# Kernel optimization log

Hardware: AMD Instinct MI355X
Metric: run time of the kernel (lower is better)

## Reference

```python
import jax, jax.numpy as jnp
import numpy as np

GROUPS = 32
EPS = 1e-5


def setup_inputs() -> dict:
    key = jax.random.key(0)
    ks = jax.random.split(key, 6)
    B, H, W, C = 2, 64, 64, 512
    wscale = 0.02  # keep logits in a sane range for softmax
    return {
        "x": jax.random.normal(ks[0], (B, H, W, C), dtype=jnp.float32),
        "gamma": jnp.ones((C,), jnp.float32),
        "beta": jnp.zeros((C,), jnp.float32),
        "wq": jax.random.normal(ks[1], (C, C), dtype=jnp.float32) * wscale,
        "bq": jnp.zeros((C,), jnp.float32),
        "wk": jax.random.normal(ks[2], (C, C), dtype=jnp.float32) * wscale,
        "bk": jnp.zeros((C,), jnp.float32),
        "wv": jax.random.normal(ks[3], (C, C), dtype=jnp.float32) * wscale,
        "bv": jnp.zeros((C,), jnp.float32),
        "wp": jax.random.normal(ks[4], (C, C), dtype=jnp.float32) * wscale,
        "bp": jnp.zeros((C,), jnp.float32),
    }


def _group_norm(x, gamma, beta):
    B, H, W, C = x.shape
    xg = x.reshape(B, H, W, GROUPS, C // GROUPS)
    mean = xg.mean(axis=(1, 2, 4), keepdims=True)
    var = xg.var(axis=(1, 2, 4), keepdims=True)
    xn = ((xg - mean) * jax.lax.rsqrt(var + EPS)).reshape(B, H, W, C)
    return xn * gamma + beta


def reference(x, gamma, beta, wq, bq, wk, bk, wv, bv, wp, bp):
    B, H, W, C = x.shape
    xn = _group_norm(x, gamma, beta)
    # 1x1 convs == per-pixel linear layers
    q = (xn @ wq + bq).reshape(B, H * W, C)
    k = (xn @ wk + bk).reshape(B, H * W, C)
    v = (xn @ wv + bv).reshape(B, H * W, C)
    scale = C ** (-0.5)
    attn = jax.nn.softmax(jnp.einsum("bqc,bkc->bqk", q, k) * scale, axis=-1)
    out = jnp.einsum("bqk,bkc->bqc", attn, v).reshape(B, H, W, C)
    return (out @ wp + bp) + x
```

## Files before the change

### kernel.cpp

```cpp
#include <hip/hip_runtime.h>


typedef __bf16 bf16_t;
typedef __bf16 bf16x8 __attribute__((ext_vector_type(8)));
typedef __bf16 bf16x4 __attribute__((ext_vector_type(4)));
typedef float  f32x4  __attribute__((ext_vector_type(4)));

__device__ __forceinline__ bf16x8 ld8(const bf16_t* p) {
    return *reinterpret_cast<const bf16x8*>(p);
}
__device__ __forceinline__ f32x4 mfma16(bf16x8 a, bf16x8 b, f32x4 c) {
    return __builtin_amdgcn_mfma_f32_16x16x32_bf16(a, b, c, 0, 0, 0);
}
__device__ __forceinline__ void gload16(const bf16_t* gp, bf16_t* lp) {
    __builtin_amdgcn_global_load_lds(
        (const __attribute__((address_space(1))) void*)gp,
        (__attribute__((address_space(3))) void*)lp, 16, 0, 0);
}

#define NPIX 8192
#define C512 512
#define SEQ  4096
#define QSCALE 0.044194173824159216f

__global__ __launch_bounds__(256) void gn_sum_k(const float* __restrict__ x,
                                                float* __restrict__ accum) {
    int bg    = blockIdx.x >> 3;
    int slice = blockIdx.x & 7;
    int b = bg >> 5, g = bg & 31;
    const float* xp = x + (size_t)b * SEQ * C512 + g * 16;
    float s = 0.f, s2 = 0.f;
    #pragma unroll
    for (int pp = 0; pp < 2; pp++) {
        int p = slice * 512 + pp * 256 + threadIdx.x;
        const float4* q = reinterpret_cast<const float4*>(xp + (size_t)p * C512);
        #pragma unroll
        for (int i = 0; i < 4; i++) {
            float4 v = q[i];
            s  += v.x + v.y + v.z + v.w;
            s2 += v.x*v.x + v.y*v.y + v.z*v.z + v.w*v.w;
        }
    }
    #pragma unroll
    for (int off = 32; off >= 1; off >>= 1) {
        s  += __shfl_down(s, off);
        s2 += __shfl_down(s2, off);
    }
    __shared__ float rs[4], rs2[4];
    int wave = threadIdx.x >> 6;
    if ((threadIdx.x & 63) == 0) { rs[wave] = s; rs2[wave] = s2; }
    __syncthreads();
    if (threadIdx.x == 0) {
        float S = rs[0] + rs[1] + rs[2] + rs[3];
        float S2 = rs2[0] + rs2[1] + rs2[2] + rs2[3];
        atomicAdd(&accum[bg * 2],     S);
        atomicAdd(&accum[bg * 2 + 1], S2);
    }
}

__global__ __launch_bounds__(256) void wt_conv_k(const float* wq, const float* wk,
                                                 const float* wv, const float* wp,
                                                 bf16_t* wqkvT, bf16_t* wpT) {
    int y = blockIdx.y;
    const float* w = (y == 0) ? wq : (y == 1) ? wk : (y == 2) ? wv : wp;
    float scale = (y == 0) ? QSCALE : 1.0f;
    int tid = blockIdx.x * 256 + threadIdx.x;
    int n = tid >> 9, k = tid & 511;
    bf16_t val = (bf16_t)(w[(size_t)k * C512 + n] * scale);
    if (y < 3) wqkvT[((size_t)y * C512 + n) * C512 + k] = val;
    else       wpT[(size_t)n * C512 + k] = val;
}

__global__ __launch_bounds__(256) void bias_merge_k(const float* bq, const float* bk,
                                                    const float* bv, float* bqkv) {
    int i = blockIdx.x * 256 + threadIdx.x;
    float v = (i < 512) ? bq[i] * QSCALE : (i < 1024) ? bk[i - 512] : bv[i - 1024];
    bqkv[i] = v;
}

__global__ __launch_bounds__(256) void xn_k(const float* __restrict__ x,
                                            const float* __restrict__ accum,
                                            const float* __restrict__ gamma,
                                            const float* __restrict__ beta,
                                            bf16_t* __restrict__ xn) {
    size_t idx = ((size_t)blockIdx.x * 256 + threadIdx.x) * 4;
    int c = (int)(idx & 511);
    size_t pix = idx >> 9;
    int b = (int)(pix >> 12);
    int g = c >> 4;
    float sum = accum[(b * 32 + g) * 2];
    float ssq = accum[(b * 32 + g) * 2 + 1];
    float mean = sum * (1.f / 65536.f);
    float var  = ssq * (1.f / 65536.f) - mean * mean;
    float rstd = rsqrtf(var + 1e-5f);
    float4 v  = *reinterpret_cast<const float4*>(x + idx);
    float4 gm = *reinterpret_cast<const float4*>(gamma + c);
    float4 bt = *reinterpret_cast<const float4*>(beta + c);
    bf16x4 o;
    o[0] = (bf16_t)((v.x - mean) * rstd * gm.x + bt.x);
    o[1] = (bf16_t)((v.y - mean) * rstd * gm.y + bt.y);
    o[2] = (bf16_t)((v.z - mean) * rstd * gm.z + bt.z);
    o[3] = (bf16_t)((v.w - mean) * rstd * gm.w + bt.w);
    *reinterpret_cast<bf16x4*>(xn + idx) = o;
}

template <int MODE>
__global__ __launch_bounds__(256, 2) void gemm128_k(
        const bf16_t* __restrict__ Aall, const bf16_t* __restrict__ Ball,
        const float* __restrict__ bias, const float* __restrict__ resid,
        void* __restrict__ out0, void* __restrict__ out1,
        void* __restrict__ out2, void* __restrict__ out3,
        float* __restrict__ lsum) {
    constexpr int TM  = (MODE == 3) ? 64 : 128;
    constexpr int ASZ = TM * 32;
    constexpr int ACH = TM / 16;
    constexpr int CPW = (ACH + 8) / 4;
    constexpr int MI  = TM / 32;
    __shared__ bf16_t smem[2 * ASZ + 8192];

    int lane = threadIdx.x & 63;
    int w    = threadIdx.x >> 6;
    int wr   = w >> 1, wc = w & 1;
    int lrow = lane & 15, quad = lane >> 4;
    int bz   = blockIdx.z;

    const bf16_t* A;
    const bf16_t* B;
    size_t lda, ldb;
    int ksteps, kofs = 0, zb = bz, sp = 0;
    if (MODE == 0)      { A = Aall;                         B = Ball;                        lda = 512;  ldb = 512;  ksteps = 16; }
    else if (MODE == 1) { A = Aall + (size_t)bz*SEQ*C512;   B = Ball + (size_t)bz*SEQ*C512;  lda = 512;  ldb = 512;  ksteps = 16; }
    else if (MODE == 2) { zb = bz >> 2; sp = bz & 3;
                          A = Aall + (size_t)zb*SEQ*SEQ;    B = Ball + (size_t)zb*C512*SEQ;  lda = SEQ;  ldb = SEQ;  ksteps = 32; kofs = sp * 1024; }
    else                { A = Aall;                         B = Ball;                        lda = 512;  ldb = 512;  ksteps = 16; }

    int bm = blockIdx.x * TM, bn = blockIdx.y * 128;

    auto stage = [&](int buf, int ks) {
        size_t k0 = (size_t)kofs + (size_t)ks * 32;
        #pragma unroll
        for (int ii = 0; ii < CPW; ii++) {
            int c = w * CPW + ii;
            if (c < ACH) {
                const bf16_t* gpA = A + (size_t)(bm + c * 16 + lrow) * lda + k0 + quad * 8;
                gload16(gpA, &smem[buf * ASZ + c * 512]);
            } else {
                int cb = c - ACH;
                const bf16_t* gpB = B + (size_t)(bn + cb * 16 + lrow) * ldb + k0 + quad * 8;
                gload16(gpB, &smem[2 * ASZ + buf * 4096 + cb * 512]);
            }
        }
    };

    f32x4 acc[MI][4] = {};

    stage(0, 0);

    for (int ks = 0; ks < ksteps; ks++) {
        int cur = ks & 1;
        __syncthreads();
        if (ks + 1 < ksteps) stage(1 - cur, ks + 1);

        const bf16_t* al = &smem[cur * ASZ + (wr * MI) * 512];
        const bf16_t* bl = &smem[2 * ASZ + cur * 4096 + (wc * 4) * 512];
        bf16x8 af[MI], bf[4];
        #pragma unroll
        for (int m = 0; m < MI; m++) af[m] = ld8(al + m * 512 + lane * 8);
        #pragma unroll
        for (int n = 0; n < 4; n++) bf[n] = ld8(bl + n * 512 + lane * 8);
        #pragma unroll
        for (int m = 0; m < MI; m++)
            #pragma unroll
            for (int n = 0; n < 4; n++)
                acc[m][n] = mfma16(af[m], bf[n], acc[m][n]);
    }

    float rs[MI][4];
    if (MODE == 1) {
        #pragma unroll
        for (int m = 0; m < MI; m++)
            #pragma unroll
            for (int i = 0; i < 4; i++) rs[m][i] = 0.f;
    }

    #pragma unroll
    for (int m = 0; m < MI; m++) {
        int rowb = bm + wr * (TM / 2) + m * 16 + quad * 4;
        #pragma unroll
        for (int n = 0; n < 4; n++) {
            int col = bn + wc * 64 + n * 16 + lrow;
            #pragma unroll
            for (int i = 0; i < 4; i++) {
                int row = rowb + i;
                float v = acc[m][n][i];
                if (MODE == 0) {
                    int seg = col >> 9, c = col & 511;
                    bf16_t val = (bf16_t)(v + bias[col]);
                    if (seg == 0) {
                        ((bf16_t*)out0)[(size_t)row * C512 + c] = val;
                    } else if (seg == 1) {
                        ((bf16_t*)out1)[(size_t)row * C512 + c] = val;
                    } else {
                        int b = row >> 12, s = row & 4095;
                        ((bf16_t*)out2)[((size_t)(b * C512 + c)) * SEQ + s] = val;
                    }
                } else if (MODE == 1) {
                    float p = __expf(fminf(v, 20.0f));
                    bf16_t* P = (bf16_t*)out0 + (size_t)bz * SEQ * SEQ;
                    P[(size_t)row * SEQ + col] = (bf16_t)p;
                    rs[m][i] += p;
                } else if (MODE == 2) {
                    bf16_t* Ops = (bf16_t*)((sp == 0) ? out0 : (sp == 1) ? out1
                                          : (sp == 2) ? out2 : out3);
                    Ops[((size_t)zb * SEQ + row) * C512 + col] = (bf16_t)v;
                } else {
                    size_t idx = (size_t)row * C512 + col;
                    ((float*)out0)[idx] = v + bias[col] + resid[idx];
                }
            }
        }
    }

    if (MODE == 1) {
        #pragma unroll
        for (int m = 0; m < MI; m++) {
            #pragma unroll
            for (int i = 0; i < 4; i++) {
                float r = rs[m][i];
                r += __shfl_xor(r, 1);
                r += __shfl_xor(r, 2);
                r += __shfl_xor(r, 4);
                r += __shfl_xor(r, 8);
                if (lrow == 0) {
                    int row = bm + wr * 64 + m * 16 + quad * 4 + i;
                    atomicAdd(&lsum[(size_t)bz * SEQ + row], r);
                }
            }
        }
    }
}

__global__ __launch_bounds__(256) void attn_combine_k(const bf16_t* __restrict__ Op0,
                                                      const bf16_t* __restrict__ Op1,
                                                      const bf16_t* __restrict__ Op2,
                                                      const bf16_t* __restrict__ Op3,
                                                      const float* __restrict__ lsum,
                                                      bf16_t* __restrict__ O) {
    int idx = blockIdx.x * 256 + threadIdx.x;
    int row = idx >> 6;
    int c8  = (idx & 63) << 3;
    float inv = 1.0f / lsum[row];
    size_t base = (size_t)row * C512 + c8;
    bf16x8 o0 = ld8(Op0 + base), o1 = ld8(Op1 + base);
    bf16x8 o2 = ld8(Op2 + base), o3 = ld8(Op3 + base);
    bf16x8 o;
    #pragma unroll
    for (int j = 0; j < 8; j++)
        o[j] = (bf16_t)(((float)o0[j] + (float)o1[j] +
                         (float)o2[j] + (float)o3[j]) * inv);
    *reinterpret_cast<bf16x8*>(O + base) = o;
}

extern "C" void kernel_launch(void* const* d_in, const int* in_sizes, int n_in,
                              void* d_out, int out_size, void* d_ws, size_t ws_size,
                              hipStream_t stream) {
    const float* x     = (const float*)d_in[0];
    const float* gamma = (const float*)d_in[1];
    const float* beta  = (const float*)d_in[2];
    const float* wq = (const float*)d_in[3];  const float* bq = (const float*)d_in[4];
    const float* wk = (const float*)d_in[5];  const float* bk = (const float*)d_in[6];
    const float* wv = (const float*)d_in[7];  const float* bv = (const float*)d_in[8];
    const float* wp = (const float*)d_in[9];  const float* bp = (const float*)d_in[10];
    float* out = (float*)d_out;

    char* ws = (char*)d_ws;
    size_t off = 0;
    float*  bqkv   = (float*)(ws + off);   off += 1536 * sizeof(float);
    float*  lsum   = (float*)(ws + off);   off += (size_t)NPIX * sizeof(float);
    float*  accum  = (float*)(ws + off);   off += 128 * sizeof(float);
    bf16_t* xn     = (bf16_t*)(ws + off);  off += (size_t)NPIX * C512 * 2;
    bf16_t* wqkvT  = (bf16_t*)(ws + off);  off += (size_t)3 * C512 * C512 * 2;
    bf16_t* wpT    = (bf16_t*)(ws + off);  off += (size_t)C512 * C512 * 2;
    bf16_t* Qb     = (bf16_t*)(ws + off);  off += (size_t)NPIX * C512 * 2;
    bf16_t* Kb     = (bf16_t*)(ws + off);  off += (size_t)NPIX * C512 * 2;
    bf16_t* VTb    = (bf16_t*)(ws + off);  off += (size_t)NPIX * C512 * 2;
    bf16_t* Op2    = (bf16_t*)(ws + off);  off += (size_t)NPIX * C512 * 2;
    bf16_t* Op3    = (bf16_t*)(ws + off);  off += (size_t)NPIX * C512 * 2;
    bf16_t* P      = (bf16_t*)(ws + off);  off += (size_t)2 * SEQ * SEQ * 2;
    bf16_t* Ob  = xn;
    bf16_t* Op0 = Qb;
    bf16_t* Op1 = Kb;

    hipMemsetAsync(lsum, 0, (size_t)(NPIX + 128) * sizeof(float), stream);

    gn_sum_k<<<512, 256, 0, stream>>>(x, accum);
    wt_conv_k<<<dim3(1024, 4), 256, 0, stream>>>(wq, wk, wv, wp, wqkvT, wpT);
    bias_merge_k<<<6, 256, 0, stream>>>(bq, bk, bv, bqkv);
    xn_k<<<4096, 256, 0, stream>>>(x, accum, gamma, beta, xn);

    gemm128_k<0><<<dim3(64, 12, 1), 256, 0, stream>>>(
        xn, wqkvT, bqkv, nullptr, Qb, Kb, VTb, nullptr, nullptr);

    gemm128_k<1><<<dim3(32, 32, 2), 256, 0, stream>>>(
        Qb, Kb, nullptr, nullptr, P, nullptr, nullptr, nullptr, lsum);

    gemm128_k<2><<<dim3(32, 4, 8), 256, 0, stream>>>(
        P, VTb, nullptr, nullptr, Op0, Op1, Op2, Op3, nullptr);

    attn_combine_k<<<2048, 256, 0, stream>>>(Op0, Op1, Op2, Op3, lsum, Ob);

    gemm128_k<3><<<dim3(128, 4, 1), 256, 0, stream>>>(
        Ob, wpT, bp, x, out, nullptr, nullptr, nullptr, nullptr);
}
```

Before: 309.5 us.

## Fuse QK^T, exp and PV into a flash-style attention kernel with key split

Replaces the separate QK^T GEMM (writing exp scores to a 64MB P buffer) and the split-K PV GEMM with one fused kernel that keeps each 64-query tile's scores in LDS and multiplies them directly by V. Keys are split in two halves across blocks, and the combine step now sums two partials instead of four. Blocks are mapped to XCDs by batch and key half. This removes the large P write and read round trip through HBM. In exchange, the grid is only 256 blocks of 512 threads with one block per CU, each holding 16 Q fragments in registers, so parallelism and latency hiding are limited.

```diff
diff --git a/kernel.cpp b/kernel.cpp
--- a/kernel.cpp
+++ b/kernel.cpp
@@ -122,22 +122,16 @@
     int w    = threadIdx.x >> 6;
     int wr   = w >> 1, wc = w & 1;
     int lrow = lane & 15, quad = lane >> 4;
-    int bz   = blockIdx.z;
-
-    const bf16_t* A;
-    const bf16_t* B;
-    size_t lda, ldb;
-    int ksteps, kofs = 0, zb = bz, sp = 0;
-    if (MODE == 0)      { A = Aall;                         B = Ball;                        lda = 512;  ldb = 512;  ksteps = 16; }
-    else if (MODE == 1) { A = Aall + (size_t)bz*SEQ*C512;   B = Ball + (size_t)bz*SEQ*C512;  lda = 512;  ldb = 512;  ksteps = 16; }
-    else if (MODE == 2) { zb = bz >> 2; sp = bz & 3;
-                          A = Aall + (size_t)zb*SEQ*SEQ;    B = Ball + (size_t)zb*C512*SEQ;  lda = SEQ;  ldb = SEQ;  ksteps = 32; kofs = sp * 1024; }
-    else                { A = Aall;                         B = Ball;                        lda = 512;  ldb = 512;  ksteps = 16; }
+
+    const bf16_t* A = Aall;
+    const bf16_t* B = Ball;
+    size_t lda = 512, ldb = 512;
+    int ksteps = 16;
 
     int bm = blockIdx.x * TM, bn = blockIdx.y * 128;
 
     auto stage = [&](int buf, int ks) {
-        size_t k0 = (size_t)kofs + (size_t)ks * 32;
+        size_t k0 = (size_t)ks * 32;
         #pragma unroll
         for (int ii = 0; ii < CPW; ii++) {
             int c = w * CPW + ii;
@@ -173,14 +167,6 @@
             #pragma unroll
             for (int n = 0; n < 4; n++)
                 acc[m][n] = mfma16(af[m], bf[n], acc[m][n]);
-    }
-
-    float rs[MI][4];
-    if (MODE == 1) {
-        #pragma unroll
-        for (int m = 0; m < MI; m++)
-            #pragma unroll
-            for (int i = 0; i < 4; i++) rs[m][i] = 0.f;
     }
 
     #pragma unroll
@@ -204,15 +190,6 @@
                         int b = row >> 12, s = row & 4095;
                         ((bf16_t*)out2)[((size_t)(b * C512 + c)) * SEQ + s] = val;
                     }
-                } else if (MODE == 1) {
-                    float p = __expf(fminf(v, 20.0f));
-                    bf16_t* P = (bf16_t*)out0 + (size_t)bz * SEQ * SEQ;
-                    P[(size_t)row * SEQ + col] = (bf16_t)p;
-                    rs[m][i] += p;
-                } else if (MODE == 2) {
-                    bf16_t* Ops = (bf16_t*)((sp == 0) ? out0 : (sp == 1) ? out1
-                                          : (sp == 2) ? out2 : out3);
-                    Ops[((size_t)zb * SEQ + row) * C512 + col] = (bf16_t)v;
                 } else {
                     size_t idx = (size_t)row * C512 + col;
                     ((float*)out0)[idx] = v + bias[col] + resid[idx];
@@ -220,44 +197,133 @@
             }
         }
     }
-
-    if (MODE == 1) {
-        #pragma unroll
-        for (int m = 0; m < MI; m++) {
+}
+
+__global__ __launch_bounds__(512, 1) void fattn_k(
+        const bf16_t* __restrict__ Q, const bf16_t* __restrict__ K,
+        const bf16_t* __restrict__ VT, bf16_t* __restrict__ Op0,
+        bf16_t* __restrict__ Op1, float* __restrict__ lsum) {
+    __shared__ bf16_t Kl[2][32 * 512];
+    __shared__ bf16_t Vl[2][512 * 32];
+    __shared__ bf16_t Pl[64 * 32];
+
+    int bid = blockIdx.x;
+    int xcd = bid & 7, loc = bid >> 3;
+    int b   = (xcd >> 1) & 1;
+    int kv  = xcd & 1;
+    int q0  = ((xcd >> 2) * 32 + loc) * 64;
+    int key0 = kv * 2048;
+
+    const bf16_t* Qb = Q  + (size_t)b * SEQ * C512;
+    const bf16_t* Kb = K  + (size_t)b * SEQ * C512;
+    const bf16_t* Vb = VT + (size_t)b * C512 * SEQ;
+    bf16_t* Op = kv ? Op1 : Op0;
+
+    int lane = threadIdx.x & 63;
+    int w    = threadIdx.x >> 6;
+    int lrow = lane & 15, quad = lane >> 4;
+    int qt = w & 3, kt = w >> 2;
+
+    bf16x8 qf[16];
+    const bf16_t* qp = Qb + (size_t)(q0 + qt * 16 + lrow) * C512 + quad * 8;
+    #pragma unroll
+    for (int ks = 0; ks < 16; ks++) qf[ks] = ld8(qp + ks * 32);
+
+    auto stage = [&](int buf, int t) {
+        #pragma unroll
+        for (int ii = 0; ii < 8; ii++) {
+            int cc = w * 8 + ii;
+            if (cc < 32) {
+                int ks = cc >> 1, ktc = cc & 1;
+                const bf16_t* gp = Kb +
+                    (size_t)(key0 + t * 32 + ktc * 16 + lrow) * C512 + ks * 32 + quad * 8;
+                gload16(gp, &Kl[buf][cc * 512]);
+            } else {
+                int ct = cc - 32;
+                const bf16_t* gp = Vb +
+                    (size_t)(ct * 16 + lrow) * SEQ + key0 + t * 32 + quad * 8;
+                gload16(gp, &Vl[buf][ct * 512]);
+            }
+        }
+    };
+
+    f32x4 oacc[4][4] = {};
+    float rs[4] = {0.f, 0.f, 0.f, 0.f};
+
+    stage(0, 0);
+
+    for (int t = 0; t < 64; t++) {
+        int cur = t & 1;
+        __syncthreads();
+        if (t < 63) stage(cur ^ 1, t + 1);
+
+        f32x4 sa = {0.f, 0.f, 0.f, 0.f};
+        #pragma unroll
+        for (int ks = 0; ks < 16; ks++) {
+            bf16x8 bf = ld8(&Kl[cur][(ks * 2 + kt) * 512 + lane * 8]);
+            sa = mfma16(qf[ks], bf, sa);
+        }
+        #pragma unroll
+        for (int i = 0; i < 4; i++) {
+            float p = __expf(fminf(sa[i], 20.0f));
+            rs[i] += p;
+            int off = qt * 512 + (quad * 4 + i) * 8 +
+                      (kt * 2 + (lrow >> 3)) * 128 + (lrow & 7);
+            Pl[off] = (bf16_t)p;
+        }
+        asm volatile("s_waitcnt lgkmcnt(0)" ::: "memory");
+        __builtin_amdgcn_s_barrier();
+        __builtin_amdgcn_sched_barrier(0);
+
+        bf16x8 pa[4];
+        #pragma unroll
+        for (int m = 0; m < 4; m++) pa[m] = ld8(&Pl[m * 512 + lane * 8]);
+        #pragma unroll
+        for (int n = 0; n < 4; n++) {
+            bf16x8 vf = ld8(&Vl[cur][(w * 4 + n) * 512 + lane * 8]);
             #pragma unroll
-            for (int i = 0; i < 4; i++) {
-                float r = rs[m][i];
-                r += __shfl_xor(r, 1);
-                r += __shfl_xor(r, 2);
-                r += __shfl_xor(r, 4);
-                r += __shfl_xor(r, 8);
-                if (lrow == 0) {
-                    int row = bm + wr * 64 + m * 16 + quad * 4 + i;
-                    atomicAdd(&lsum[(size_t)bz * SEQ + row], r);
-                }
-            }
-        }
-    }
-}
-
-__global__ __launch_bounds__(256) void attn_combine_k(const bf16_t* __restrict__ Op0,
-                                                      const bf16_t* __restrict__ Op1,
-                                                      const bf16_t* __restrict__ Op2,
-                                                      const bf16_t* __restrict__ Op3,
-                                                      const float* __restrict__ lsum,
-                                                      bf16_t* __restrict__ O) {
+            for (int m = 0; m < 4; m++)
+                oacc[m][n] = mfma16(pa[m], vf, oacc[m][n]);
+        }
+    }
+
+    #pragma unroll
+    for (int i = 0; i < 4; i++) {
+        float r = rs[i];
+        r += __shfl_xor(r, 1);
+        r += __shfl_xor(r, 2);
+        r += __shfl_xor(r, 4);
+        r += __shfl_xor(r, 8);
+        if (lrow == 0)
+            atomicAdd(&lsum[(size_t)b * SEQ + q0 + qt * 16 + quad * 4 + i], r);
+    }
+
+    #pragma unroll
+    for (int m = 0; m < 4; m++) {
+        int row = q0 + m * 16 + quad * 4;
+        #pragma unroll
+        for (int n = 0; n < 4; n++) {
+            int col = w * 64 + n * 16 + lrow;
+            #pragma unroll
+            for (int i = 0; i < 4; i++)
+                Op[((size_t)b * SEQ + row + i) * C512 + col] = (bf16_t)oacc[m][n][i];
+        }
+    }
+}
+
+__global__ __launch_bounds__(256) void attn_combine2_k(
+        const bf16_t* __restrict__ Op0, const bf16_t* __restrict__ Op1,
+        const float* __restrict__ lsum, bf16_t* __restrict__ O) {
     int idx = blockIdx.x * 256 + threadIdx.x;
     int row = idx >> 6;
     int c8  = (idx & 63) << 3;
     float inv = 1.0f / lsum[row];
     size_t base = (size_t)row * C512 + c8;
     bf16x8 o0 = ld8(Op0 + base), o1 = ld8(Op1 + base);
-    bf16x8 o2 = ld8(Op2 + base), o3 = ld8(Op3 + base);
     bf16x8 o;
     #pragma unroll
     for (int j = 0; j < 8; j++)
-        o[j] = (bf16_t)(((float)o0[j] + (float)o1[j] +
-                         (float)o2[j] + (float)o3[j]) * inv);
+        o[j] = (bf16_t)(((float)o0[j] + (float)o1[j]) * inv);
     *reinterpret_cast<bf16x8*>(O + base) = o;
 }
 
@@ -284,12 +350,9 @@
     bf16_t* Qb     = (bf16_t*)(ws + off);  off += (size_t)NPIX * C512 * 2;
     bf16_t* Kb     = (bf16_t*)(ws + off);  off += (size_t)NPIX * C512 * 2;
     bf16_t* VTb    = (bf16_t*)(ws + off);  off += (size_t)NPIX * C512 * 2;
-    bf16_t* Op2    = (bf16_t*)(ws + off);  off += (size_t)NPIX * C512 * 2;
-    bf16_t* Op3    = (bf16_t*)(ws + off);  off += (size_t)NPIX * C512 * 2;
-    bf16_t* P      = (bf16_t*)(ws + off);  off += (size_t)2 * SEQ * SEQ * 2;
+    bf16_t* Op0    = (bf16_t*)(ws + off);  off += (size_t)NPIX * C512 * 2;
+    bf16_t* Op1    = (bf16_t*)(ws + off);  off += (size_t)NPIX * C512 * 2;
     bf16_t* Ob  = xn;
-    bf16_t* Op0 = Qb;
-    bf16_t* Op1 = Kb;
 
     hipMemsetAsync(lsum, 0, (size_t)(NPIX + 128) * sizeof(float), stream);
 
@@ -301,13 +364,9 @@
     gemm128_k<0><<<dim3(64, 12, 1), 256, 0, stream>>>(
         xn, wqkvT, bqkv, nullptr, Qb, Kb, VTb, nullptr, nullptr);
 
-    gemm128_k<1><<<dim3(32, 32, 2), 256, 0, stream>>>(
-        Qb, Kb, nullptr, nullptr, P, nullptr, nullptr, nullptr, lsum);
-
-    gemm128_k<2><<<dim3(32, 4, 8), 256, 0, stream>>>(
-        P, VTb, nullptr, nullptr, Op0, Op1, Op2, Op3, nullptr);
-
-    attn_combine_k<<<2048, 256, 0, stream>>>(Op0, Op1, Op2, Op3, lsum, Ob);
+    fattn_k<<<256, 512, 0, stream>>>(Qb, Kb, VTb, Op0, Op1, lsum);
+
+    attn_combine2_k<<<2048, 256, 0, stream>>>(Op0, Op1, lsum, Ob);
 
     gemm128_k<3><<<dim3(128, 4, 1), 256, 0, stream>>>(
         Ob, wpT, bp, x, out, nullptr, nullptr, nullptr, nullptr);
```

Measured after the change: 305.3 us. About the same (-1.3%).
